# Optimization experiments

Measured on AMD Instinct MI355X. Metric: run time of the kernel, lower is better.

## Reference

```python
import jax, jax.numpy as jnp
import numpy as np

B, C, D_IN, D_H, D_QK = 64, 512, 1024, 1024, 512
EPS = 1e-5


def setup_inputs() -> dict:
    key = jax.random.key(0)
    ks = jax.random.split(key, 24)
    din2 = D_IN + D_H  # concat([x, h]) feature dim
    s_qk = 1.0 / np.sqrt(din2)
    inp = {
        "x": jax.random.normal(ks[0], (B, C, D_IN), jnp.float32),
        "h": jax.random.normal(ks[1], (B, C, D_H), jnp.float32),
    }
    i = 2
    for g in ("r", "z", "n"):
        inp[f"Wq_{g}"] = jax.random.normal(ks[i], (din2, D_QK), jnp.float32) * s_qk; i += 1
        inp[f"bq_{g}"] = jnp.zeros((D_QK,), jnp.float32)
        inp[f"Wk_{g}"] = jax.random.normal(ks[i], (din2, D_QK), jnp.float32) * s_qk; i += 1
        inp[f"bk_{g}"] = jnp.zeros((D_QK,), jnp.float32)
        inp[f"Wv_{g}"] = jax.random.normal(ks[i], (din2, D_H), jnp.float32) * s_qk; i += 1
        inp[f"bv_{g}"] = jnp.zeros((D_H,), jnp.float32)
    inp["gamma"] = jnp.ones((D_H,), jnp.float32)
    inp["beta"] = jnp.zeros((D_H,), jnp.float32)
    return inp


def _self_attention(xin, Wq, bq, Wk, bk, Wv, bv):
    # xin: (B, C, 2D) ; attention over channel axis C
    Q = xin @ Wq + bq            # (B, C, d_qk)
    K = xin @ Wk + bk            # (B, C, d_qk)
    V = xin @ Wv + bv            # (B, C, d_h)
    scale = 1.0 / jnp.sqrt(jnp.asarray(Q.shape[-1], jnp.float32))
    scores = jnp.einsum("bcd,bed->bce", Q, K) * scale   # (B, C, C)
    attn = jax.nn.softmax(scores, axis=-1)
    return jnp.einsum("bce,bed->bcd", attn, V)          # (B, C, d_h)


def reference(x, h,
              Wq_r, bq_r, Wk_r, bk_r, Wv_r, bv_r,
              Wq_z, bq_z, Wk_z, bk_z, Wv_z, bv_z,
              Wq_n, bq_n, Wk_n, bk_n, Wv_n, bv_n,
              gamma, beta):
    xh = jnp.concatenate([x, h], axis=2)
    r = _self_attention(xh, Wq_r, bq_r, Wk_r, bk_r, Wv_r, bv_r)
    z = _self_attention(xh, Wq_z, bq_z, Wk_z, bk_z, Wv_z, bv_z)
    reset = jax.nn.sigmoid(r)
    update = jax.nn.sigmoid(z)
    xhr = jnp.concatenate([x, h * reset], axis=2)
    n = _self_attention(xhr, Wq_n, bq_n, Wk_n, bk_n, Wv_n, bv_n)
    new_state = (1.0 - update) * h + update * jnp.tanh(n)
    # LayerNorm over last dim
    mu = jnp.mean(new_state, axis=-1, keepdims=True)
    var = jnp.var(new_state, axis=-1, keepdims=True)
    return (new_state - mu) * jax.lax.rsqrt(var + EPS) * gamma + beta
```

## Files before the change

### kernel.cpp

```cpp
#include <hip/hip_runtime.h>
#include <math.h>

typedef __attribute__((ext_vector_type(8))) short short8;
typedef __attribute__((ext_vector_type(4))) float f32x4;

#define EPI_QKV   0
#define EPI_PEXP  1
#define EPI_R     2
#define EPI_Z     3
#define EPI_N     4

__device__ __forceinline__ unsigned short f2bf(float f) {
    unsigned int u = __float_as_uint(f);
    u += 0x7fffu + ((u >> 16) & 1u);
    return (unsigned short)(u >> 16);
}
__device__ __forceinline__ float bf2f(unsigned short s) {
    return __uint_as_float(((unsigned int)s) << 16);
}

struct alignas(8) us4 { unsigned short a, b, c, d; };

#define GLD_LDS16(gp, lp) \
    __builtin_amdgcn_global_load_lds((const __attribute__((address_space(1))) unsigned int*)(gp), \
                                     (__attribute__((address_space(3))) unsigned int*)(lp), 16, 0, 0)

#define BAR   do { asm volatile("" ::: "memory"); __builtin_amdgcn_s_barrier(); \
                   asm volatile("" ::: "memory"); } while (0)
#define VMC0  asm volatile("s_waitcnt vmcnt(0)" ::: "memory")

template<int EPI, int SWZ>
__global__ void __launch_bounds__(512, 2)
gemm256(const unsigned short* __restrict__ A, long long sAb, int lda,
        const unsigned short* __restrict__ Bt, long long sBb, int ldb,
        const float* __restrict__ bias,
        void* __restrict__ C, long long sCb, int ldc,
        int K, float scale,
        const float* __restrict__ hptr,
        const unsigned short* __restrict__ updptr,
        float* __restrict__ psum,
        unsigned short* __restrict__ vt)
{
    extern __shared__ char smem[];

    const int z = blockIdx.z;
    A  += (size_t)z * (size_t)sAb;
    Bt += (size_t)z * (size_t)sBb;

    int bx, by;
    if (SWZ) {
        const int bid = blockIdx.y * 8 + blockIdx.x;
        const int xcd = bid & 7, i = bid >> 3;
        bx = i & 7;
        by = (xcd << 4) | (i >> 3);
    } else {
        bx = blockIdx.x; by = blockIdx.y;
    }
    const int m0 = by * 256;
    const int n0 = bx * 256;

    const int tid = threadIdx.x;
    const int w  = tid >> 6;
    const int l  = tid & 63;
    const int wr = w >> 2;
    const int wc = w & 3;
    const int lr = l & 15;
    const int lg = l >> 4;
    const int rs = (lr & 7) << 4;

    const int srw = l >> 3;
    const int scb = ((l & 7) << 4) ^ (srw << 4);

    const long long ldab = (long long)lda * 2;
    const long long ldbb = (long long)ldb * 2;

    f32x4 acc[2][4][4] = {};
    short8 a[4][2], b[4][2];

#define STAGE1(gbase, ldbytes, grow0, ldsoff) { \
    const char* g_ = (const char*)(gbase) + \
        (size_t)((grow0) + w*8 + srw) * (ldbytes) + scb; \
    GLD_LDS16(g_, smem + (ldsoff) + (w << 10)); }

#define AOFF(buf) ((buf)*65536)
#define BOFF(buf) ((buf)*65536 + 32768)

#define SA(buf, base) { STAGE1(base, ldab, m0 + 0,   AOFF(buf) + 0); \
                        STAGE1(base, ldab, m0 + 64,  AOFF(buf) + 8192); \
                        STAGE1(base, ldab, m0 + 128, AOFF(buf) + 16384); \
                        STAGE1(base, ldab, m0 + 192, AOFF(buf) + 24576); }
#define SB(buf, base) { STAGE1(base, ldbb, n0 + 0,   BOFF(buf) + 0); \
                        STAGE1(base, ldbb, n0 + 64,  BOFF(buf) + 8192); \
                        STAGE1(base, ldbb, n0 + 128, BOFF(buf) + 16384); \
                        STAGE1(base, ldbb, n0 + 192, BOFF(buf) + 24576); }

#define LDA8(MH, buf) { \
    const char* Ab_ = smem + AOFF(buf); \
    _Pragma("unroll") \
    for (int mf = 0; mf < 4; ++mf) { \
        const int row_ = wr*128 + (MH)*64 + mf*16 + lr; \
        _Pragma("unroll") \
        for (int kk = 0; kk < 2; ++kk) \
            a[mf][kk] = *(const short8*)(Ab_ + row_*128 + ((kk*64 + lg*16) ^ rs)); } }

#define LDB4(BH, buf) { \
    const char* Bb_ = smem + BOFF(buf); \
    _Pragma("unroll") \
    for (int nf = 0; nf < 2; ++nf) { \
        const int row_ = wc*64 + (BH)*32 + nf*16 + lr; \
        _Pragma("unroll") \
        for (int kk = 0; kk < 2; ++kk) \
            b[(BH)*2+nf][kk] = *(const short8*)(Bb_ + row_*128 + ((kk*64 + lg*16) ^ rs)); } }

#define MMA16(MH, BH) { \
    __builtin_amdgcn_s_setprio(1); \
    _Pragma("unroll") \
    for (int kk = 0; kk < 2; ++kk) \
    _Pragma("unroll") \
    for (int mf = 0; mf < 4; ++mf) \
    _Pragma("unroll") \
    for (int nf = 0; nf < 2; ++nf) \
        acc[MH][mf][(BH)*2+nf] = __builtin_amdgcn_mfma_f32_16x16x32_bf16( \
            a[mf][kk], b[(BH)*2+nf][kk], acc[MH][mf][(BH)*2+nf], 0, 0, 0); \
    __builtin_amdgcn_s_setprio(0); }

    SA(0, A); SB(0, Bt);
    VMC0;
    BAR;

    const int NT = K >> 6;
    for (int t = 0; t < NT; ++t) {
        const int p = t & 1, q = p ^ 1;
        const bool s1 = (t + 1 < NT);
        const unsigned short* Anx = A  + (size_t)(t + 1) * 64;
        const unsigned short* Bnx = Bt + (size_t)(t + 1) * 64;

        if (s1) { SA(q, Anx); SB(q, Bnx); }
        LDA8(0, p); LDB4(0, p); LDB4(1, p);
        MMA16(0, 0); MMA16(0, 1);
        LDA8(1, p);
        MMA16(1, 0); MMA16(1, 1);
        VMC0;
        BAR;
    }

    const int Mb = gridDim.y << 8;
    const size_t zc = (size_t)z * (size_t)sCb;

    if (EPI == EPI_PEXP) {
        float psl[2][4][4];
        #pragma unroll
        for (int mh = 0; mh < 2; ++mh)
            #pragma unroll
            for (int mf = 0; mf < 4; ++mf)
                #pragma unroll
                for (int r = 0; r < 4; ++r) psl[mh][mf][r] = 0.0f;

        #pragma unroll
        for (int mh = 0; mh < 2; ++mh)
        #pragma unroll
        for (int mf = 0; mf < 4; ++mf)
        #pragma unroll
        for (int nf = 0; nf < 4; ++nf) {
            const int col = n0 + wc * 64 + nf * 16 + lr;
            #pragma unroll
            for (int r = 0; r < 4; ++r) {
                const int row = m0 + wr * 128 + mh * 64 + mf * 16 + lg * 4 + r;
                const float e = __expf(acc[mh][mf][nf][r] * scale);
                ((unsigned short*)C)[zc + (size_t)row * ldc + col] = f2bf(e);
                psl[mh][mf][r] += e;
            }
        }
        #pragma unroll
        for (int d = 1; d < 16; d <<= 1)
            #pragma unroll
            for (int mh = 0; mh < 2; ++mh)
                #pragma unroll
                for (int mf = 0; mf < 4; ++mf)
                    #pragma unroll
                    for (int r = 0; r < 4; ++r)
                        psl[mh][mf][r] += __shfl_xor(psl[mh][mf][r], d);
        __syncthreads();
        float* red = (float*)smem;
        if (lr == 0) {
            #pragma unroll
            for (int mh = 0; mh < 2; ++mh)
                #pragma unroll
                for (int mf = 0; mf < 4; ++mf)
                    #pragma unroll
                    for (int r = 0; r < 4; ++r)
                        red[wc * 256 + wr * 128 + mh * 64 + mf * 16 + lg * 4 + r]
                            = psl[mh][mf][r];
        }
        __syncthreads();
        if (tid < 256) {
            const float sres = red[tid] + red[256 + tid] + red[512 + tid] + red[768 + tid];
            psum[(size_t)bx * 32768 + (size_t)z * 512 + m0 + tid] = sres;
        }
        return;
    }

    float invs[2][4][4];
    if (EPI == EPI_R || EPI == EPI_Z || EPI == EPI_N) {
        #pragma unroll
        for (int mh = 0; mh < 2; ++mh)
            #pragma unroll
            for (int mf = 0; mf < 4; ++mf)
                #pragma unroll
                for (int r = 0; r < 4; ++r) {
                    const int row = m0 + wr * 128 + mh * 64 + mf * 16 + lg * 4 + r;
                    const size_t gr = (size_t)z * 512 + row;
                    invs[mh][mf][r] = 1.0f / (psum[gr] + psum[32768 + gr]);
                }
    }

    #pragma unroll
    for (int mh = 0; mh < 2; ++mh) {
        #pragma unroll
        for (int mf = 0; mf < 4; ++mf) {
            #pragma unroll
            for (int nf = 0; nf < 4; ++nf) {
                const int col = n0 + wc * 64 + nf * 16 + lr;
                const float bval = (EPI == EPI_QKV) ? bias[col] : 0.0f;
                if (EPI == EPI_QKV && bx >= 4) {
                    const int row0 = m0 + wr * 128 + mh * 64 + mf * 16 + lg * 4;
                    us4 o = { f2bf(acc[mh][mf][nf][0] + bval),
                              f2bf(acc[mh][mf][nf][1] + bval),
                              f2bf(acc[mh][mf][nf][2] + bval),
                              f2bf(acc[mh][mf][nf][3] + bval) };
                    *(us4*)(vt + (size_t)(row0 >> 9) * 524288 +
                            (size_t)(col - 1024) * 512 + (row0 & 511)) = o;
                } else {
                    #pragma unroll
                    for (int r = 0; r < 4; ++r) {
                        const int row = m0 + wr * 128 + mh * 64 + mf * 16 + lg * 4 + r;
                        float v = acc[mh][mf][nf][r] + bval;
                        if (EPI == EPI_QKV) {
                            ((unsigned short*)C)[(size_t)row * ldc + col] = f2bf(v);
                        } else if (EPI == EPI_R) {
                            v *= invs[mh][mf][r];
                            const size_t flat = (size_t)z * Mb + row;
                            const float hh = hptr[flat * 1024 + col];
                            const float sg = 1.0f / (1.0f + __expf(-v));
                            ((unsigned short*)C)[flat * 2048 + 1024 + col] = f2bf(hh * sg);
                        } else if (EPI == EPI_Z) {
                            v *= invs[mh][mf][r];
                            const size_t flat = (size_t)z * Mb + row;
                            const float sg = 1.0f / (1.0f + __expf(-v));
                            ((unsigned short*)C)[flat * 1024 + col] = f2bf(sg);
                        } else {
                            v *= invs[mh][mf][r];
                            const size_t flat = (size_t)z * Mb + row;
                            const float u  = bf2f(updptr[flat * 1024 + col]);
                            const float hh = hptr[flat * 1024 + col];
                            ((float*)C)[flat * 1024 + col] = (1.0f - u) * hh + u * tanhf(v);
                        }
                    }
                }
            }
        }
    }
#undef STAGE1
#undef AOFF
#undef BOFF
#undef SA
#undef SB
#undef LDA8
#undef LDB4
#undef MMA16
}


__global__ void __launch_bounds__(256)
prep_xh(const float* __restrict__ x, const float* __restrict__ h, unsigned short* __restrict__ xh)
{
    const size_t t = (size_t)blockIdx.x * 256 + threadIdx.x;
    const size_t f = t * 4;
    const size_t row = f >> 10, col = f & 1023;
    const float4 vx = *(const float4*)(x + f);
    const float4 vh = *(const float4*)(h + f);
    us4 ox = { f2bf(vx.x), f2bf(vx.y), f2bf(vx.z), f2bf(vx.w) };
    us4 oh = { f2bf(vh.x), f2bf(vh.y), f2bf(vh.z), f2bf(vh.w) };
    *(us4*)(xh + row * 2048 + col)        = ox;
    *(us4*)(xh + row * 2048 + 1024 + col) = oh;
}

__global__ void __launch_bounds__(256)
transpose_w(const float* __restrict__ W, unsigned short* __restrict__ WT, int N)
{
    __shared__ float t[32][33];
    const int k0 = blockIdx.y * 32, n0 = blockIdx.x * 32;
    const int tx = threadIdx.x & 31, ty = threadIdx.x >> 5;
    #pragma unroll
    for (int i = 0; i < 4; ++i)
        t[ty + i * 8][tx] = W[(size_t)(k0 + ty + i * 8) * N + n0 + tx];
    __syncthreads();
    #pragma unroll
    for (int i = 0; i < 4; ++i)
        WT[(size_t)(n0 + ty + i * 8) * 2048 + k0 + tx] = f2bf(t[tx][ty + i * 8]);
}

__global__ void __launch_bounds__(256)
layernorm1024(float* __restrict__ Y, const float* __restrict__ gamma, const float* __restrict__ beta)
{
    const int row = blockIdx.x * 4 + (threadIdx.x >> 6);
    const int l = threadIdx.x & 63;
    float* p = Y + (size_t)row * 1024;
    float4 v[4];
    float s = 0.0f, s2 = 0.0f;
    #pragma unroll
    for (int i = 0; i < 4; ++i) {
        v[i] = ((const float4*)p)[i * 64 + l];
        s  += v[i].x + v[i].y + v[i].z + v[i].w;
        s2 += v[i].x * v[i].x + v[i].y * v[i].y + v[i].z * v[i].z + v[i].w * v[i].w;
    }
    #pragma unroll
    for (int d = 32; d; d >>= 1) { s += __shfl_xor(s, d); s2 += __shfl_xor(s2, d); }
    const float mu = s * (1.0f / 1024.0f);
    const float var = s2 * (1.0f / 1024.0f) - mu * mu;
    const float inv = rsqrtf(var + 1e-5f);
    #pragma unroll
    for (int i = 0; i < 4; ++i) {
        const float4 gv = ((const float4*)gamma)[i * 64 + l];
        const float4 bv = ((const float4*)beta)[i * 64 + l];
        float4 o;
        o.x = (v[i].x - mu) * inv * gv.x + bv.x;
        o.y = (v[i].y - mu) * inv * gv.y + bv.y;
        o.z = (v[i].z - mu) * inv * gv.z + bv.z;
        o.w = (v[i].w - mu) * inv * gv.w + bv.w;
        ((float4*)p)[i * 64 + l] = o;
    }
}

__global__ void __launch_bounds__(256)
concat_bias(const float* __restrict__ a, const float* __restrict__ b,
            const float* __restrict__ c, float* __restrict__ o)
{
    const int i = blockIdx.x * 256 + threadIdx.x;
    o[i] = (i < 512) ? a[i] : (i < 1024) ? b[i - 512] : c[i - 1024];
}

extern "C" void kernel_launch(void* const* d_in, const int* in_sizes, int n_in,
                              void* d_out, int out_size, void* d_ws, size_t ws_size,
                              hipStream_t stream)
{
    (void)in_sizes; (void)n_in; (void)out_size; (void)ws_size;

    const float* x = (const float*)d_in[0];
    const float* h = (const float*)d_in[1];
    const float* Wf[9]; const float* bia[9];
    for (int g = 0; g < 3; ++g)
        for (int j = 0; j < 3; ++j) {
            Wf[g * 3 + j]  = (const float*)d_in[2 + g * 6 + j * 2];
            bia[g * 3 + j] = (const float*)d_in[2 + g * 6 + j * 2 + 1];
        }
    const float* gamma = (const float*)d_in[20];
    const float* beta  = (const float*)d_in[21];
    float* out = (float*)d_out;

    const int LDS_BYTES = 131072;
    hipFuncSetAttribute((const void*)gemm256<EPI_QKV, 1>,  hipFuncAttributeMaxDynamicSharedMemorySize, LDS_BYTES);
    hipFuncSetAttribute((const void*)gemm256<EPI_PEXP, 0>, hipFuncAttributeMaxDynamicSharedMemorySize, LDS_BYTES);
    hipFuncSetAttribute((const void*)gemm256<EPI_R, 0>,    hipFuncAttributeMaxDynamicSharedMemorySize, LDS_BYTES);
    hipFuncSetAttribute((const void*)gemm256<EPI_Z, 0>,    hipFuncAttributeMaxDynamicSharedMemorySize, LDS_BYTES);
    hipFuncSetAttribute((const void*)gemm256<EPI_N, 0>,    hipFuncAttributeMaxDynamicSharedMemorySize, LDS_BYTES);

    char* ws = (char*)d_ws;
    size_t off = 0;
    auto alloc = [&](size_t bytes) -> void* {
        void* p = ws + off; off += (bytes + 255) & ~(size_t)255; return p;
    };
    unsigned short* xh  = (unsigned short*)alloc((size_t)32768 * 2048 * 2);
    unsigned short* WT  = (unsigned short*)alloc((size_t)12582912 * 2);
    unsigned short* QK  = (unsigned short*)alloc((size_t)32768 * 1024 * 2);
    unsigned short* Vt  = (unsigned short*)alloc((size_t)32768 * 1024 * 2);
    unsigned short* Pb  = (unsigned short*)alloc((size_t)64 * 512 * 512 * 2);
    unsigned short* upd = (unsigned short*)alloc((size_t)32768 * 1024 * 2);
    float*          psb = (float*)alloc((size_t)2 * 32768 * 4);
    float*          bct = (float*)alloc((size_t)3 * 2048 * 4);

    size_t wtoff[9];
    {
        size_t o = 0;
        for (int g = 0; g < 3; ++g) {
            wtoff[g * 3 + 0] = o; o += (size_t)512 * 2048;
            wtoff[g * 3 + 1] = o; o += (size_t)512 * 2048;
            wtoff[g * 3 + 2] = o; o += (size_t)1024 * 2048;
        }
    }

    prep_xh<<<32768, 256, 0, stream>>>(x, h, xh);
    for (int i = 0; i < 9; ++i) {
        const int N = (i % 3 == 2) ? 1024 : 512;
        transpose_w<<<dim3(N / 32, 64, 1), 256, 0, stream>>>(Wf[i], WT + wtoff[i], N);
    }
    for (int g = 0; g < 3; ++g)
        concat_bias<<<8, 256, 0, stream>>>(bia[g * 3 + 0], bia[g * 3 + 1], bia[g * 3 + 2], bct + g * 2048);

    const float scscale = 0.044194173824159216f;

    auto gate = [&](int g, int epi) {
        const unsigned short* wT = WT + wtoff[g * 3 + 0];
        gemm256<EPI_QKV, 1><<<dim3(8, 128, 1), 512, LDS_BYTES, stream>>>(
            xh, 0, 2048, wT, 0, 2048, bct + g * 2048,
            QK, 0, 1024, 2048, 0.0f, nullptr, nullptr, nullptr, Vt);
        gemm256<EPI_PEXP, 0><<<dim3(2, 2, 64), 512, LDS_BYTES, stream>>>(
            QK, 524288, 1024, QK + 512, 524288, 1024, nullptr,
            Pb, 262144, 512, 512, scscale, nullptr, nullptr, psb, nullptr);
        if (epi == EPI_Z)
            gemm256<EPI_Z, 0><<<dim3(4, 2, 64), 512, LDS_BYTES, stream>>>(
                Pb, 262144, 512, Vt, 524288, 512, nullptr,
                upd, 0, 1024, 512, 0.0f, nullptr, nullptr, psb, nullptr);
        else if (epi == EPI_R)
            gemm256<EPI_R, 0><<<dim3(4, 2, 64), 512, LDS_BYTES, stream>>>(
                Pb, 262144, 512, Vt, 524288, 512, nullptr,
                xh, 0, 2048, 512, 0.0f, h, nullptr, psb, nullptr);
        else
            gemm256<EPI_N, 0><<<dim3(4, 2, 64), 512, LDS_BYTES, stream>>>(
                Pb, 262144, 512, Vt, 524288, 512, nullptr,
                out, 0, 1024, 512, 0.0f, h, upd, psb, nullptr);
    };

    gate(1, EPI_Z);
    gate(0, EPI_R);
    gate(2, EPI_N);
    layernorm1024<<<8192, 256, 0, stream>>>(out, gamma, beta);
}
```

Measured before the change: 1.308 ms.

## Load GEMM B operand directly from global into registers, bypassing LDS

The B tile is no longer staged through LDS with global_load_lds. Each wave now reads its B fragments straight from global memory into registers. The next tile's B loads are placed between the MFMA groups so they overlap with compute, and the dynamic LDS request drops from 128KB to 64KB, which may allow more blocks per CU. The cost is that waves sharing a column slice load the same B data redundantly, using less-coalesced 16-byte per-lane global reads that depend on cache hits, and registers must hold data in flight.

After: 1.922 ms. +46.9%, slower.

```diff
diff --git a/kernel.cpp b/kernel.cpp
--- a/kernel.cpp
+++ b/kernel.cpp
@@ -82,17 +82,21 @@
         (size_t)((grow0) + w*8 + srw) * (ldbytes) + scb; \
     GLD_LDS16(g_, smem + (ldsoff) + (w << 10)); }
 
-#define AOFF(buf) ((buf)*65536)
-#define BOFF(buf) ((buf)*65536 + 32768)
+#define AOFF(buf) ((buf) << 15)
 
 #define SA(buf, base) { STAGE1(base, ldab, m0 + 0,   AOFF(buf) + 0); \
                         STAGE1(base, ldab, m0 + 64,  AOFF(buf) + 8192); \
                         STAGE1(base, ldab, m0 + 128, AOFF(buf) + 16384); \
                         STAGE1(base, ldab, m0 + 192, AOFF(buf) + 24576); }
-#define SB(buf, base) { STAGE1(base, ldbb, n0 + 0,   BOFF(buf) + 0); \
-                        STAGE1(base, ldbb, n0 + 64,  BOFF(buf) + 8192); \
-                        STAGE1(base, ldbb, n0 + 128, BOFF(buf) + 16384); \
-                        STAGE1(base, ldbb, n0 + 192, BOFF(buf) + 24576); }
+
+#define BLOADH(BH, kt) { \
+    _Pragma("unroll") \
+    for (int nf = 0; nf < 2; ++nf) { \
+        const int row_ = n0 + wc*64 + (BH)*32 + nf*16 + lr; \
+        const char* gb_ = (const char*)Bt + (size_t)row_ * ldbb + (size_t)(kt) * 2; \
+        _Pragma("unroll") \
+        for (int kk = 0; kk < 2; ++kk) \
+            b[(BH)*2+nf][kk] = *(const short8*)(gb_ + kk*64 + lg*16); } }
 
 #define LDA8(MH, buf) { \
     const char* Ab_ = smem + AOFF(buf); \
@@ -102,15 +106,6 @@
         _Pragma("unroll") \
         for (int kk = 0; kk < 2; ++kk) \
             a[mf][kk] = *(const short8*)(Ab_ + row_*128 + ((kk*64 + lg*16) ^ rs)); } }
-
-#define LDB4(BH, buf) { \
-    const char* Bb_ = smem + BOFF(buf); \
-    _Pragma("unroll") \
-    for (int nf = 0; nf < 2; ++nf) { \
-        const int row_ = wc*64 + (BH)*32 + nf*16 + lr; \
-        _Pragma("unroll") \
-        for (int kk = 0; kk < 2; ++kk) \
-            b[(BH)*2+nf][kk] = *(const short8*)(Bb_ + row_*128 + ((kk*64 + lg*16) ^ rs)); } }
 
 #define MMA16(MH, BH) { \
     __builtin_amdgcn_s_setprio(1); \
@@ -124,7 +119,8 @@
             a[mf][kk], b[(BH)*2+nf][kk], acc[MH][mf][(BH)*2+nf], 0, 0, 0); \
     __builtin_amdgcn_s_setprio(0); }
 
-    SA(0, A); SB(0, Bt);
+    SA(0, A);
+    BLOADH(0, 0); BLOADH(1, 0);
     VMC0;
     BAR;
 
@@ -132,14 +128,17 @@
     for (int t = 0; t < NT; ++t) {
         const int p = t & 1, q = p ^ 1;
         const bool s1 = (t + 1 < NT);
-        const unsigned short* Anx = A  + (size_t)(t + 1) * 64;
-        const unsigned short* Bnx = Bt + (size_t)(t + 1) * 64;
-
-        if (s1) { SA(q, Anx); SB(q, Bnx); }
-        LDA8(0, p); LDB4(0, p); LDB4(1, p);
+        const unsigned short* Anx = A + (size_t)(t + 1) * 64;
+        const int ktn = (t + 1) << 6;
+
+        if (s1) { SA(q, Anx); }
+        LDA8(0, p);
         MMA16(0, 0); MMA16(0, 1);
         LDA8(1, p);
-        MMA16(1, 0); MMA16(1, 1);
+        MMA16(1, 0);
+        if (s1) { BLOADH(0, ktn); }
+        MMA16(1, 1);
+        if (s1) { BLOADH(1, ktn); }
         VMC0;
         BAR;
     }
@@ -262,11 +261,9 @@
     }
 #undef STAGE1
 #undef AOFF
-#undef BOFF
 #undef SA
-#undef SB
+#undef BLOADH
 #undef LDA8
-#undef LDB4
 #undef MMA16
 }
 
@@ -358,7 +355,7 @@
     const float* beta  = (const float*)d_in[21];
     float* out = (float*)d_out;
 
-    const int LDS_BYTES = 131072;
+    const int LDS_BYTES = 65536;
     hipFuncSetAttribute((const void*)gemm256<EPI_QKV, 1>,  hipFuncAttributeMaxDynamicSharedMemorySize, LDS_BYTES);
     hipFuncSetAttribute((const void*)gemm256<EPI_PEXP, 0>, hipFuncAttributeMaxDynamicSharedMemorySize, LDS_BYTES);
     hipFuncSetAttribute((const void*)gemm256<EPI_R, 0>,    hipFuncAttributeMaxDynamicSharedMemorySize, LDS_BYTES);
```

## Shrink GEMM tile to 128x256 with BK=32 and drop LDS swizzle

Applied to the files above, without the earlier changes.

Replaces the 256x256x64 GEMM tile with a 128x256x32 tile, shrinking LDS from 128KB to 48KB and raising the launch-bounds occupancy hint from 2 to 4 blocks. The grids double in M to match, and the XCD swizzle is updated. The aim is more resident waves and better latency hiding. The cost is half the per-block data reuse, twice as many barriers per K, and the loss of the XOR LDS swizzle, so 64-byte row strides may cause bank conflicts.

After: 1.458 ms. 1.11x slower.

```diff
diff --git a/kernel.cpp b/kernel.cpp
--- a/kernel.cpp
+++ b/kernel.cpp
@@ -30,8 +30,8 @@
 #define VMC0  asm volatile("s_waitcnt vmcnt(0)" ::: "memory")
 
 template<int EPI, int SWZ>
-__global__ void __launch_bounds__(512, 2)
-gemm256(const unsigned short* __restrict__ A, long long sAb, int lda,
+__global__ void __launch_bounds__(512, 4)
+gemm128(const unsigned short* __restrict__ A, long long sAb, int lda,
         const unsigned short* __restrict__ Bt, long long sBb, int ldb,
         const float* __restrict__ bias,
         void* __restrict__ C, long long sCb, int ldc,
@@ -52,11 +52,11 @@
         const int bid = blockIdx.y * 8 + blockIdx.x;
         const int xcd = bid & 7, i = bid >> 3;
         bx = i & 7;
-        by = (xcd << 4) | (i >> 3);
+        by = (xcd << 5) + (i >> 3);
     } else {
         bx = blockIdx.x; by = blockIdx.y;
     }
-    const int m0 = by * 256;
+    const int m0 = by * 128;
     const int n0 = bx * 256;
 
     const int tid = threadIdx.x;
@@ -66,206 +66,174 @@
     const int wc = w & 3;
     const int lr = l & 15;
     const int lg = l >> 4;
-    const int rs = (lr & 7) << 4;
-
-    const int srw = l >> 3;
-    const int scb = ((l & 7) << 4) ^ (srw << 4);
 
     const long long ldab = (long long)lda * 2;
     const long long ldbb = (long long)ldb * 2;
 
-    f32x4 acc[2][4][4] = {};
-    short8 a[4][2], b[4][2];
-
-#define STAGE1(gbase, ldbytes, grow0, ldsoff) { \
-    const char* g_ = (const char*)(gbase) + \
-        (size_t)((grow0) + w*8 + srw) * (ldbytes) + scb; \
-    GLD_LDS16(g_, smem + (ldsoff) + (w << 10)); }
-
-#define AOFF(buf) ((buf)*65536)
-#define BOFF(buf) ((buf)*65536 + 32768)
-
-#define SA(buf, base) { STAGE1(base, ldab, m0 + 0,   AOFF(buf) + 0); \
-                        STAGE1(base, ldab, m0 + 64,  AOFF(buf) + 8192); \
-                        STAGE1(base, ldab, m0 + 128, AOFF(buf) + 16384); \
-                        STAGE1(base, ldab, m0 + 192, AOFF(buf) + 24576); }
-#define SB(buf, base) { STAGE1(base, ldbb, n0 + 0,   BOFF(buf) + 0); \
-                        STAGE1(base, ldbb, n0 + 64,  BOFF(buf) + 8192); \
-                        STAGE1(base, ldbb, n0 + 128, BOFF(buf) + 16384); \
-                        STAGE1(base, ldbb, n0 + 192, BOFF(buf) + 24576); }
-
-#define LDA8(MH, buf) { \
+    f32x4 acc[4][4] = {};
+    short8 a[4], b[4];
+
+#define AOFF(buf) ((buf) * 8192)
+#define BOFF(buf) (16384 + (buf) * 16384)
+
+#define SA(buf, base) { \
+    const char* g_ = (const char*)(base) + (size_t)(m0 + (tid >> 2)) * ldab + ((tid & 3) << 4); \
+    GLD_LDS16(g_, smem + AOFF(buf) + ((w << 10) + (l << 4))); }
+
+#define SB(buf, base) { \
+    _Pragma("unroll") \
+    for (int j = 0; j < 2; ++j) { \
+        const char* g_ = (const char*)(base) + \
+            (size_t)(n0 + j * 128 + (tid >> 2)) * ldbb + ((tid & 3) << 4); \
+        GLD_LDS16(g_, smem + BOFF(buf) + j * 8192 + ((w << 10) + (l << 4))); } }
+
+#define LDA4(buf) { \
     const char* Ab_ = smem + AOFF(buf); \
     _Pragma("unroll") \
-    for (int mf = 0; mf < 4; ++mf) { \
-        const int row_ = wr*128 + (MH)*64 + mf*16 + lr; \
-        _Pragma("unroll") \
-        for (int kk = 0; kk < 2; ++kk) \
-            a[mf][kk] = *(const short8*)(Ab_ + row_*128 + ((kk*64 + lg*16) ^ rs)); } }
-
-#define LDB4(BH, buf) { \
+    for (int mf = 0; mf < 4; ++mf) \
+        a[mf] = *(const short8*)(Ab_ + (wr * 64 + mf * 16 + lr) * 64 + lg * 16); }
+
+#define LDB4(buf) { \
     const char* Bb_ = smem + BOFF(buf); \
     _Pragma("unroll") \
-    for (int nf = 0; nf < 2; ++nf) { \
-        const int row_ = wc*64 + (BH)*32 + nf*16 + lr; \
-        _Pragma("unroll") \
-        for (int kk = 0; kk < 2; ++kk) \
-            b[(BH)*2+nf][kk] = *(const short8*)(Bb_ + row_*128 + ((kk*64 + lg*16) ^ rs)); } }
-
-#define MMA16(MH, BH) { \
+    for (int nf = 0; nf < 4; ++nf) \
+        b[nf] = *(const short8*)(Bb_ + (wc * 64 + nf * 16 + lr) * 64 + lg * 16); }
+
+#define MMA16() { \
     __builtin_amdgcn_s_setprio(1); \
     _Pragma("unroll") \
-    for (int kk = 0; kk < 2; ++kk) \
-    _Pragma("unroll") \
     for (int mf = 0; mf < 4; ++mf) \
     _Pragma("unroll") \
-    for (int nf = 0; nf < 2; ++nf) \
-        acc[MH][mf][(BH)*2+nf] = __builtin_amdgcn_mfma_f32_16x16x32_bf16( \
-            a[mf][kk], b[(BH)*2+nf][kk], acc[MH][mf][(BH)*2+nf], 0, 0, 0); \
+    for (int nf = 0; nf < 4; ++nf) \
+        acc[mf][nf] = __builtin_amdgcn_mfma_f32_16x16x32_bf16( \
+            a[mf], b[nf], acc[mf][nf], 0, 0, 0); \
     __builtin_amdgcn_s_setprio(0); }
 
     SA(0, A); SB(0, Bt);
     VMC0;
     BAR;
 
-    const int NT = K >> 6;
+    const int NT = K >> 5;
     for (int t = 0; t < NT; ++t) {
         const int p = t & 1, q = p ^ 1;
         const bool s1 = (t + 1 < NT);
-        const unsigned short* Anx = A  + (size_t)(t + 1) * 64;
-        const unsigned short* Bnx = Bt + (size_t)(t + 1) * 64;
-
-        if (s1) { SA(q, Anx); SB(q, Bnx); }
-        LDA8(0, p); LDB4(0, p); LDB4(1, p);
-        MMA16(0, 0); MMA16(0, 1);
-        LDA8(1, p);
-        MMA16(1, 0); MMA16(1, 1);
+        const unsigned short* An = A  + (size_t)(t + 1) * 32;
+        const unsigned short* Bn = Bt + (size_t)(t + 1) * 32;
+
+        if (s1) { SA(q, An); SB(q, Bn); }
+        LDA4(p); LDB4(p);
+        MMA16();
         VMC0;
         BAR;
     }
 
-    const int Mb = gridDim.y << 8;
+    const int Mb = gridDim.y << 7;
     const size_t zc = (size_t)z * (size_t)sCb;
 
     if (EPI == EPI_PEXP) {
-        float psl[2][4][4];
-        #pragma unroll
-        for (int mh = 0; mh < 2; ++mh)
+        float psl[4][4];
+        #pragma unroll
+        for (int mf = 0; mf < 4; ++mf)
+            #pragma unroll
+            for (int r = 0; r < 4; ++r) psl[mf][r] = 0.0f;
+
+        #pragma unroll
+        for (int mf = 0; mf < 4; ++mf)
+        #pragma unroll
+        for (int nf = 0; nf < 4; ++nf) {
+            const int col = n0 + wc * 64 + nf * 16 + lr;
+            #pragma unroll
+            for (int r = 0; r < 4; ++r) {
+                const int row = m0 + wr * 64 + mf * 16 + lg * 4 + r;
+                const float e = __expf(acc[mf][nf][r] * scale);
+                ((unsigned short*)C)[zc + (size_t)row * ldc + col] = f2bf(e);
+                psl[mf][r] += e;
+            }
+        }
+        #pragma unroll
+        for (int d = 1; d < 16; d <<= 1)
             #pragma unroll
             for (int mf = 0; mf < 4; ++mf)
                 #pragma unroll
-                for (int r = 0; r < 4; ++r) psl[mh][mf][r] = 0.0f;
-
-        #pragma unroll
-        for (int mh = 0; mh < 2; ++mh)
-        #pragma unroll
-        for (int mf = 0; mf < 4; ++mf)
-        #pragma unroll
-        for (int nf = 0; nf < 4; ++nf) {
-            const int col = n0 + wc * 64 + nf * 16 + lr;
-            #pragma unroll
-            for (int r = 0; r < 4; ++r) {
-                const int row = m0 + wr * 128 + mh * 64 + mf * 16 + lg * 4 + r;
-                const float e = __expf(acc[mh][mf][nf][r] * scale);
-                ((unsigned short*)C)[zc + (size_t)row * ldc + col] = f2bf(e);
-                psl[mh][mf][r] += e;
-            }
-        }
-        #pragma unroll
-        for (int d = 1; d < 16; d <<= 1)
-            #pragma unroll
-            for (int mh = 0; mh < 2; ++mh)
-                #pragma unroll
-                for (int mf = 0; mf < 4; ++mf)
-                    #pragma unroll
-                    for (int r = 0; r < 4; ++r)
-                        psl[mh][mf][r] += __shfl_xor(psl[mh][mf][r], d);
+                for (int r = 0; r < 4; ++r)
+                    psl[mf][r] += __shfl_xor(psl[mf][r], d);
         __syncthreads();
         float* red = (float*)smem;
         if (lr == 0) {
             #pragma unroll
-            for (int mh = 0; mh < 2; ++mh)
-                #pragma unroll
-                for (int mf = 0; mf < 4; ++mf)
-                    #pragma unroll
-                    for (int r = 0; r < 4; ++r)
-                        red[wc * 256 + wr * 128 + mh * 64 + mf * 16 + lg * 4 + r]
-                            = psl[mh][mf][r];
-        }
-        __syncthreads();
-        if (tid < 256) {
-            const float sres = red[tid] + red[256 + tid] + red[512 + tid] + red[768 + tid];
-            psum[(size_t)bx * 32768 + (size_t)z * 512 + m0 + tid] = sres;
-        }
-        return;
-    }
-
-    float invs[2][4][4];
-    if (EPI == EPI_R || EPI == EPI_Z || EPI == EPI_N) {
-        #pragma unroll
-        for (int mh = 0; mh < 2; ++mh)
-            #pragma unroll
             for (int mf = 0; mf < 4; ++mf)
                 #pragma unroll
+                for (int r = 0; r < 4; ++r)
+                    red[wc * 128 + wr * 64 + mf * 16 + lg * 4 + r] = psl[mf][r];
+        }
+        __syncthreads();
+        if (tid < 128) {
+            const float sres = red[tid] + red[128 + tid] + red[256 + tid] + red[384 + tid];
+            psum[(size_t)bx * 32768 + (size_t)z * 512 + m0 + tid] = sres;
+        }
+        return;
+    }
+
+    float invs[4][4];
+    if (EPI == EPI_R || EPI == EPI_Z || EPI == EPI_N) {
+        #pragma unroll
+        for (int mf = 0; mf < 4; ++mf)
+            #pragma unroll
+            for (int r = 0; r < 4; ++r) {
+                const int row = m0 + wr * 64 + mf * 16 + lg * 4 + r;
+                const size_t gr = (size_t)z * 512 + row;
+                invs[mf][r] = 1.0f / (psum[gr] + psum[32768 + gr]);
+            }
+    }
+
+    #pragma unroll
+    for (int mf = 0; mf < 4; ++mf) {
+        #pragma unroll
+        for (int nf = 0; nf < 4; ++nf) {
+            const int col = n0 + wc * 64 + nf * 16 + lr;
+            const float bval = (EPI == EPI_QKV) ? bias[col] : 0.0f;
+            if (EPI == EPI_QKV && bx >= 4) {
+                const int row0 = m0 + wr * 64 + mf * 16 + lg * 4;
+                us4 o = { f2bf(acc[mf][nf][0] + bval),
+                          f2bf(acc[mf][nf][1] + bval),
+                          f2bf(acc[mf][nf][2] + bval),
+                          f2bf(acc[mf][nf][3] + bval) };
+                *(us4*)(vt + (size_t)(row0 >> 9) * 524288 +
+                        (size_t)(col - 1024) * 512 + (row0 & 511)) = o;
+            } else {
+                #pragma unroll
                 for (int r = 0; r < 4; ++r) {
-                    const int row = m0 + wr * 128 + mh * 64 + mf * 16 + lg * 4 + r;
-                    const size_t gr = (size_t)z * 512 + row;
-                    invs[mh][mf][r] = 1.0f / (psum[gr] + psum[32768 + gr]);
-                }
-    }
-
-    #pragma unroll
-    for (int mh = 0; mh < 2; ++mh) {
-        #pragma unroll
-        for (int mf = 0; mf < 4; ++mf) {
-            #pragma unroll
-            for (int nf = 0; nf < 4; ++nf) {
-                const int col = n0 + wc * 64 + nf * 16 + lr;
-                const float bval = (EPI == EPI_QKV) ? bias[col] : 0.0f;
-                if (EPI == EPI_QKV && bx >= 4) {
-                    const int row0 = m0 + wr * 128 + mh * 64 + mf * 16 + lg * 4;
-                    us4 o = { f2bf(acc[mh][mf][nf][0] + bval),
-                              f2bf(acc[mh][mf][nf][1] + bval),
-                              f2bf(acc[mh][mf][nf][2] + bval),
-                              f2bf(acc[mh][mf][nf][3] + bval) };
-                    *(us4*)(vt + (size_t)(row0 >> 9) * 524288 +
-                            (size_t)(col - 1024) * 512 + (row0 & 511)) = o;
-                } else {
-                    #pragma unroll
-                    for (int r = 0; r < 4; ++r) {
-                        const int row = m0 + wr * 128 + mh * 64 + mf * 16 + lg * 4 + r;
-                        float v = acc[mh][mf][nf][r] + bval;
-                        if (EPI == EPI_QKV) {
-                            ((unsigned short*)C)[(size_t)row * ldc + col] = f2bf(v);
-                        } else if (EPI == EPI_R) {
-                            v *= invs[mh][mf][r];
-                            const size_t flat = (size_t)z * Mb + row;
-                            const float hh = hptr[flat * 1024 + col];
-                            const float sg = 1.0f / (1.0f + __expf(-v));
-                            ((unsigned short*)C)[flat * 2048 + 1024 + col] = f2bf(hh * sg);
-                        } else if (EPI == EPI_Z) {
-                            v *= invs[mh][mf][r];
-                            const size_t flat = (size_t)z * Mb + row;
-                            const float sg = 1.0f / (1.0f + __expf(-v));
-                            ((unsigned short*)C)[flat * 1024 + col] = f2bf(sg);
-                        } else {
-                            v *= invs[mh][mf][r];
-                            const size_t flat = (size_t)z * Mb + row;
-                            const float u  = bf2f(updptr[flat * 1024 + col]);
-                            const float hh = hptr[flat * 1024 + col];
-                            ((float*)C)[flat * 1024 + col] = (1.0f - u) * hh + u * tanhf(v);
-                        }
+                    const int row = m0 + wr * 64 + mf * 16 + lg * 4 + r;
+                    float v = acc[mf][nf][r] + bval;
+                    if (EPI == EPI_QKV) {
+                        ((unsigned short*)C)[(size_t)row * ldc + col] = f2bf(v);
+                    } else if (EPI == EPI_R) {
+                        v *= invs[mf][r];
+                        const size_t flat = (size_t)z * Mb + row;
+                        const float hh = hptr[flat * 1024 + col];
+                        const float sg = 1.0f / (1.0f + __expf(-v));
+                        ((unsigned short*)C)[flat * 2048 + 1024 + col] = f2bf(hh * sg);
+                    } else if (EPI == EPI_Z) {
+                        v *= invs[mf][r];
+                        const size_t flat = (size_t)z * Mb + row;
+                        const float sg = 1.0f / (1.0f + __expf(-v));
+                        ((unsigned short*)C)[flat * 1024 + col] = f2bf(sg);
+                    } else {
+                        v *= invs[mf][r];
+                        const size_t flat = (size_t)z * Mb + row;
+                        const float u  = bf2f(updptr[flat * 1024 + col]);
+                        const float hh = hptr[flat * 1024 + col];
+                        ((float*)C)[flat * 1024 + col] = (1.0f - u) * hh + u * tanhf(v);
                     }
                 }
             }
         }
     }
-#undef STAGE1
 #undef AOFF
 #undef BOFF
 #undef SA
 #undef SB
-#undef LDA8
+#undef LDA4
 #undef LDB4
 #undef MMA16
 }
@@ -358,12 +326,12 @@
     const float* beta  = (const float*)d_in[21];
     float* out = (float*)d_out;
 
-    const int LDS_BYTES = 131072;
-    hipFuncSetAttribute((const void*)gemm256<EPI_QKV, 1>,  hipFuncAttributeMaxDynamicSharedMemorySize, LDS_BYTES);
-    hipFuncSetAttribute((const void*)gemm256<EPI_PEXP, 0>, hipFuncAttributeMaxDynamicSharedMemorySize, LDS_BYTES);
-    hipFuncSetAttribute((const void*)gemm256<EPI_R, 0>,    hipFuncAttributeMaxDynamicSharedMemorySize, LDS_BYTES);
-    hipFuncSetAttribute((const void*)gemm256<EPI_Z, 0>,    hipFuncAttributeMaxDynamicSharedMemorySize, LDS_BYTES);
-    hipFuncSetAttribute((const void*)gemm256<EPI_N, 0>,    hipFuncAttributeMaxDynamicSharedMemorySize, LDS_BYTES);
+    const int LDS_BYTES = 49152;
+    hipFuncSetAttribute((const void*)gemm128<EPI_QKV, 1>,  hipFuncAttributeMaxDynamicSharedMemorySize, LDS_BYTES);
+    hipFuncSetAttribute((const void*)gemm128<EPI_PEXP, 0>, hipFuncAttributeMaxDynamicSharedMemorySize, LDS_BYTES);
+    hipFuncSetAttribute((const void*)gemm128<EPI_R, 0>,    hipFuncAttributeMaxDynamicSharedMemorySize, LDS_BYTES);
+    hipFuncSetAttribute((const void*)gemm128<EPI_Z, 0>,    hipFuncAttributeMaxDynamicSharedMemorySize, LDS_BYTES);
+    hipFuncSetAttribute((const void*)gemm128<EPI_N, 0>,    hipFuncAttributeMaxDynamicSharedMemorySize, LDS_BYTES);
 
     char* ws = (char*)d_ws;
     size_t off = 0;
@@ -401,22 +369,22 @@
 
     auto gate = [&](int g, int epi) {
         const unsigned short* wT = WT + wtoff[g * 3 + 0];
-        gemm256<EPI_QKV, 1><<<dim3(8, 128, 1), 512, LDS_BYTES, stream>>>(
+        gemm128<EPI_QKV, 1><<<dim3(8, 256, 1), 512, LDS_BYTES, stream>>>(
             xh, 0, 2048, wT, 0, 2048, bct + g * 2048,
             QK, 0, 1024, 2048, 0.0f, nullptr, nullptr, nullptr, Vt);
-        gemm256<EPI_PEXP, 0><<<dim3(2, 2, 64), 512, LDS_BYTES, stream>>>(
+        gemm128<EPI_PEXP, 0><<<dim3(2, 4, 64), 512, LDS_BYTES, stream>>>(
             QK, 524288, 1024, QK + 512, 524288, 1024, nullptr,
             Pb, 262144, 512, 512, scscale, nullptr, nullptr, psb, nullptr);
         if (epi == EPI_Z)
-            gemm256<EPI_Z, 0><<<dim3(4, 2, 64), 512, LDS_BYTES, stream>>>(
+            gemm128<EPI_Z, 0><<<dim3(4, 4, 64), 512, LDS_BYTES, stream>>>(
                 Pb, 262144, 512, Vt, 524288, 512, nullptr,
                 upd, 0, 1024, 512, 0.0f, nullptr, nullptr, psb, nullptr);
         else if (epi == EPI_R)
-            gemm256<EPI_R, 0><<<dim3(4, 2, 64), 512, LDS_BYTES, stream>>>(
+            gemm128<EPI_R, 0><<<dim3(4, 4, 64), 512, LDS_BYTES, stream>>>(
                 Pb, 262144, 512, Vt, 524288, 512, nullptr,
                 xh, 0, 2048, 512, 0.0f, h, nullptr, psb, nullptr);
         else
-            gemm256<EPI_N, 0><<<dim3(4, 2, 64), 512, LDS_BYTES, stream>>>(
+            gemm128<EPI_N, 0><<<dim3(4, 4, 64), 512, LDS_BYTES, stream>>>(
                 Pb, 262144, 512, Vt, 524288, 512, nullptr,
                 out, 0, 1024, 512, 0.0f, h, upd, psb, nullptr);
     };
```
